# Kernel tuning notes

Measured on AMD Instinct MI355X. Metric: run time of the kernel, lower is better.

Reference implementation:

```python
import jax, jax.numpy as jnp
import numpy as np

T = 4096          # total tokens across ragged segments
H = 4096          # hidden_size
I = 11008         # intermediate_size
R = 16            # lora_rank
A = 4             # number of adapters (segments)


def setup_inputs() -> dict:
    key = jax.random.key(0)
    ks = jax.random.split(key, 12)
    inp = {
        "x": jax.random.normal(ks[0], (T, H), jnp.float32),
        "gate_w": jax.random.normal(ks[1], (I, H), jnp.float32) * (1.0 / np.sqrt(H)),
        "up_w": jax.random.normal(ks[2], (I, H), jnp.float32) * (1.0 / np.sqrt(H)),
        "down_w": jax.random.normal(ks[3], (H, I), jnp.float32) * (1.0 / np.sqrt(I)),
        "gate_wa": jax.random.normal(ks[4], (A, H, R), jnp.float32) * 0.01,
        "gate_wb": jax.random.normal(ks[5], (A, R, I), jnp.float32) * 0.01,
        "up_wa": jax.random.normal(ks[6], (A, H, R), jnp.float32) * 0.01,
        "up_wb": jax.random.normal(ks[7], (A, R, I), jnp.float32) * 0.01,
        "down_wa": jax.random.normal(ks[8], (A, I, R), jnp.float32) * 0.01,
        "down_wb": jax.random.normal(ks[9], (A, R, H), jnp.float32) * 0.01,
        "seg_ids": jnp.sort(jax.random.randint(ks[10], (T,), 0, A, jnp.int32)),
    }
    return inp


def _add_lora(y, inp, wa, wb, mask):
    # Segment-batched low-rank GEMM (Punica/S-LoRA add_lora):
    # for token t in segment a:  y[t] += inp[t] @ wa[a] @ wb[a]
    # mask: [T, A] one-hot of token->adapter assignment.
    # [A, T, R]: project into rank space for every adapter (R tiny), mask out
    xa = jnp.einsum('th,ahr->tar', inp, wa) * mask[:, :, None]   # [T, A, R]
    a, r = wb.shape[0], wb.shape[1]
    # collapse (A, R) so the expansion is one GEMM, no [A, T, out] intermediate
    delta = xa.reshape(inp.shape[0], a * r) @ wb.reshape(a * r, wb.shape[2])
    return y + delta


def reference(x, gate_w, up_w, down_w, gate_wa, gate_wb, up_wa, up_wb,
              down_wa, down_wb, seg_ids):
    mask = (seg_ids[:, None] == jnp.arange(A, dtype=seg_ids.dtype)[None, :]
            ).astype(x.dtype)                                    # [T, A]
    gate = x @ gate_w.T                                          # [T, I]
    gate = _add_lora(gate, x, gate_wa, gate_wb, mask)
    gate = jax.nn.silu(gate)
    up = x @ up_w.T                                              # [T, I]
    up = _add_lora(up, x, up_wa, up_wb, mask)
    t = gate * up
    down = t @ down_w.T                                          # [T, H]
    down = _add_lora(down, t, down_wa, down_wb, mask)
    return down
```

## Files before the change

kernel.cpp:

```cpp
#include <hip/hip_runtime.h>

#define T_TOK 4096
#define HID   4096
#define IMD   11008

using f32x4  = __attribute__((ext_vector_type(4))) float;
using bf16x8 = __attribute__((ext_vector_type(8))) __bf16;
union FragCast { int4 i; bf16x8 b; };

__device__ __forceinline__ unsigned f2bf_bits(float f) {
  unsigned u = __float_as_uint(f);
  return (u + 0x7fffu + ((u >> 16) & 1u)) >> 16;
}
__device__ __forceinline__ float bf2f(short s) {
  return __uint_as_float(((unsigned)(unsigned short)s) << 16);
}
__device__ __forceinline__ int4 cvt8(const float4 f0, const float4 f1) {
  int4 r;
  r.x = f2bf_bits(f0.x) | (f2bf_bits(f0.y) << 16);
  r.y = f2bf_bits(f0.z) | (f2bf_bits(f0.w) << 16);
  r.z = f2bf_bits(f1.x) | (f2bf_bits(f1.y) << 16);
  r.w = f2bf_bits(f1.z) | (f2bf_bits(f1.w) << 16);
  return r;
}
__device__ __forceinline__ void gload16(const void* g, void* l) {
  __builtin_amdgcn_global_load_lds(
      (__attribute__((address_space(1))) void*)g,
      (__attribute__((address_space(3))) void*)l, 16, 0, 0);
}

__global__ void cvt_pad(const float* __restrict__ in, short* __restrict__ out,
                        int C8, long ldin, long ldout) {
  long r = blockIdx.x;
  const float4* s = (const float4*)(in + r * ldin);
  int4* d = (int4*)(out + r * ldout);
  for (int c = threadIdx.x; c < C8; c += blockDim.x)
    d[c] = cvt8(s[2 * c], s[2 * c + 1]);
}

__global__ void build_wbT_pad(const float* __restrict__ wb,
                              short* __restrict__ out, int N, long ldout,
                              long K) {
  int n = blockIdx.x * blockDim.x + threadIdx.x;
  int ar = blockIdx.y;
  if (n < N) out[(long)n * ldout + K + ar] = (short)f2bf_bits(wb[(long)ar * N + n]);
}

__global__ void tail_copy(const short* __restrict__ src, short* dst, long ld) {
  dst[(long)blockIdx.x * ld + threadIdx.x] = src[blockIdx.x * 64 + threadIdx.x];
}

template <int KD, int NOUT>
__global__ __launch_bounds__(256)
void lora_proj(const short* __restrict__ Abf, long ldA,
               const float* __restrict__ wa0, const float* __restrict__ wa1,
               const int* __restrict__ seg, short* out0, long ld0, short* out1,
               long ld1) {
  __shared__ __align__(16) short rowbuf[KD];
  __shared__ float part[NOUT][4][16];
  int t = blockIdx.x, tid = threadIdx.x;
  int a = seg[t];
  const int4* src = (const int4*)(Abf + (long)t * ldA);
  for (int c = tid; c < KD / 8; c += 256) ((int4*)rowbuf)[c] = src[c];
  __syncthreads();
  int w = tid >> 6, l = tid & 63;
  int r = l & 15, g = l >> 4;
  const int HW = KD / 4;
  float s0 = 0.f, s1 = 0.f;
  const float* p0 = wa0 + (long)a * KD * 16 + r;
  const float* p1 = (NOUT == 2) ? (wa1 + (long)a * KD * 16 + r) : nullptr;
  int h = w * HW + g;
  for (int k = 0; k < HW / 4; ++k, h += 4) {
    float xv = bf2f(rowbuf[h]);
    s0 = fmaf(xv, p0[(long)h * 16], s0);
    if (NOUT == 2) s1 = fmaf(xv, p1[(long)h * 16], s1);
  }
  s0 += __shfl_xor(s0, 16); s0 += __shfl_xor(s0, 32);
  if (NOUT == 2) { s1 += __shfl_xor(s1, 16); s1 += __shfl_xor(s1, 32); }
  if (l < 16) { part[0][w][r] = s0; if (NOUT == 2) part[1][w][r] = s1; }
  __syncthreads();
  if (tid < 64 * NOUT) {
    int m = tid >> 6, ar = tid & 63;
    float v = 0.f;
    if ((ar >> 4) == a) {
      int r2 = ar & 15;
      v = part[m][0][r2] + part[m][1][r2] + part[m][2][r2] + part[m][3][r2];
    }
    short b = (short)f2bf_bits(v);
    if (m == 0) out0[(long)t * ld0 + ar] = b;
    else        out1[(long)t * ld1 + ar] = b;
  }
}

template <int MODE>
__global__ __launch_bounds__(512, 2)
void gemm256(const short* __restrict__ A, const short* __restrict__ B,
             const short* gbuf, short* outB, float* outF, int nby, long ldK,
             int iters, long ldo) {
  extern __shared__ __align__(16) char smem[];

  int nwg = gridDim.x;
  int orig = blockIdx.x;
  int q = nwg >> 3, rr = nwg & 7;
  int xcd = orig & 7, loc = orig >> 3;
  int swz = (xcd < rr ? xcd * (q + 1) : rr * (q + 1) + (xcd - rr) * q) + loc;
  int by = swz % nby, bx = swz / nby;
  long row0 = (long)bx * 256, col0 = (long)by * 256;

  int tid = threadIdx.x;
  int l = tid & 63, wid = tid >> 6;
  int wr = wid >> 2, wc = wid & 3;
  int lrow = l & 15, lhi = l >> 4, md = lrow & 7;

  const short* aP[4]; const short* bP[4];
  int dst[4];
#pragma unroll
  for (int k = 0; k < 4; ++k) {
    int idx = tid + k * 512;
    int r = idx >> 3, c8 = idx & 7;
    aP[k] = A + (row0 + r) * ldK + (c8 ^ (r & 7)) * 8;
    bP[k] = B + (col0 + r) * ldK + (c8 ^ (r & 7)) * 8;
    dst[k] = idx * 16;
  }

  auto stageA = [&](int bi) {
    char* d = smem + bi * 32768;
#pragma unroll
    for (int k = 0; k < 4; ++k) { gload16(aP[k], d + dst[k]); aP[k] += 64; }
  };
  auto stageB = [&](int bi) {
    char* d = smem + 98304 + bi * 32768;
#pragma unroll
    for (int k = 0; k < 4; ++k) { gload16(bP[k], d + dst[k]); bP[k] += 64; }
  };

  f32x4 acc[8][4];
  f32x4 zr = {0.f, 0.f, 0.f, 0.f};
#pragma unroll
  for (int mi = 0; mi < 8; ++mi)
#pragma unroll
    for (int ni = 0; ni < 4; ++ni) acc[mi][ni] = zr;

  const int csel0 = (lhi ^ md) * 16;
  const int csel1 = ((4 + lhi) ^ md) * 16;

  stageA(0); stageB(0); stageA(1);
  int ca = 0, sa = 2;
  for (int t = 0; t < iters; ++t) {
    if (t + 1 < iters) asm volatile("s_waitcnt vmcnt(4)" ::: "memory");
    else               asm volatile("s_waitcnt vmcnt(0)" ::: "memory");
    asm volatile("s_barrier" ::: "memory");
    if (t + 1 < iters) stageB((t + 1) & 1);
    if (t + 2 < iters) { stageA(sa); sa = (sa == 2) ? 0 : sa + 1; }

    const char* Ab = smem + ca * 32768;
    const char* Bb = smem + 98304 + (t & 1) * 32768;
    ca = (ca == 2) ? 0 : ca + 1;

    bf16x8 bF[4][2];
#pragma unroll
    for (int ni = 0; ni < 4; ++ni) {
      const char* base = Bb + (wc * 64 + ni * 16 + lrow) * 128;
      FragCast f0, f1;
      f0.i = *(const int4*)(base + csel0);
      f1.i = *(const int4*)(base + csel1);
      bF[ni][0] = f0.b; bF[ni][1] = f1.b;
    }
#pragma unroll
    for (int qm = 0; qm < 2; ++qm) {
      bf16x8 aF[4][2];
#pragma unroll
      for (int mi = 0; mi < 4; ++mi) {
        const char* base = Ab + (wr * 128 + qm * 64 + mi * 16 + lrow) * 128;
        FragCast f0, f1;
        f0.i = *(const int4*)(base + csel0);
        f1.i = *(const int4*)(base + csel1);
        aF[mi][0] = f0.b; aF[mi][1] = f1.b;
      }
      __builtin_amdgcn_s_setprio(1);
#pragma unroll
      for (int mi = 0; mi < 4; ++mi)
#pragma unroll
        for (int ni = 0; ni < 4; ++ni) {
          acc[qm * 4 + mi][ni] = __builtin_amdgcn_mfma_f32_16x16x32_bf16(
              aF[mi][0], bF[ni][0], acc[qm * 4 + mi][ni], 0, 0, 0);
          acc[qm * 4 + mi][ni] = __builtin_amdgcn_mfma_f32_16x16x32_bf16(
              aF[mi][1], bF[ni][1], acc[qm * 4 + mi][ni], 0, 0, 0);
        }
      __builtin_amdgcn_s_setprio(0);
    }
  }

#pragma unroll
  for (int qm = 0; qm < 2; ++qm)
#pragma unroll
    for (int mi = 0; mi < 4; ++mi)
#pragma unroll
      for (int ni = 0; ni < 4; ++ni)
#pragma unroll
        for (int j = 0; j < 4; ++j) {
          long grow = row0 + wr * 128 + qm * 64 + mi * 16 + lhi * 4 + j;
          long gcol = col0 + wc * 64 + ni * 16 + lrow;
          long idx = grow * ldo + gcol;
          float v = acc[qm * 4 + mi][ni][j];
          if constexpr (MODE == 0) {
            outB[idx] = (short)f2bf_bits(v);
          } else if constexpr (MODE == 1) {
            float g = bf2f(gbuf[idx]);
            float t2 = g * (1.f / (1.f + __expf(-g))) * v;
            outB[idx] = (short)f2bf_bits(t2);
          } else {
            outF[idx] = v;
          }
        }
}

extern "C" void kernel_launch(void* const* d_in, const int* in_sizes, int n_in,
                              void* d_out, int out_size, void* d_ws,
                              size_t ws_size, hipStream_t stream) {
  const float* x       = (const float*)d_in[0];
  const float* gate_w  = (const float*)d_in[1];
  const float* up_w    = (const float*)d_in[2];
  const float* down_w  = (const float*)d_in[3];
  const float* gate_wa = (const float*)d_in[4];
  const float* gate_wb = (const float*)d_in[5];
  const float* up_wa   = (const float*)d_in[6];
  const float* up_wb   = (const float*)d_in[7];
  const float* down_wa = (const float*)d_in[8];
  const float* down_wb = (const float*)d_in[9];
  const int*   seg     = (const int*)d_in[10];

  char* ws = (char*)d_ws;
  short* xg_pad = (short*)(ws);
  short* wA     = (short*)(ws + 34078720);
  short* wB     = (short*)(ws + 125665280);
  short* t_pad  = (short*)(ws + 217251840);
  short* xa_u   = (short*)(ws + 307953664);

  const int LDS_BYTES = 163840;
  hipFuncSetAttribute(reinterpret_cast<const void*>(&gemm256<0>),
                      hipFuncAttributeMaxDynamicSharedMemorySize, LDS_BYTES);
  hipFuncSetAttribute(reinterpret_cast<const void*>(&gemm256<1>),
                      hipFuncAttributeMaxDynamicSharedMemorySize, LDS_BYTES);
  hipFuncSetAttribute(reinterpret_cast<const void*>(&gemm256<2>),
                      hipFuncAttributeMaxDynamicSharedMemorySize, LDS_BYTES);

  cvt_pad<<<T_TOK, 256, 0, stream>>>(x, xg_pad, 512, HID, 4160);
  cvt_pad<<<IMD, 256, 0, stream>>>(gate_w, wA, 512, HID, 4160);
  cvt_pad<<<IMD, 256, 0, stream>>>(up_w, wB, 512, HID, 4160);
  build_wbT_pad<<<dim3(43, 64), 256, 0, stream>>>(gate_wb, wA, IMD, 4160, HID);
  build_wbT_pad<<<dim3(43, 64), 256, 0, stream>>>(up_wb, wB, IMD, 4160, HID);
  lora_proj<HID, 2><<<T_TOK, 256, 0, stream>>>(
      xg_pad, 4160, gate_wa, up_wa, seg, xg_pad + HID, 4160, xa_u, 64);

  gemm256<0><<<16 * 43, 512, LDS_BYTES, stream>>>(
      xg_pad, wA, nullptr, t_pad, nullptr, 43, 4160, 65, 11072);
  tail_copy<<<T_TOK, 64, 0, stream>>>(xa_u, xg_pad + HID, 4160);
  gemm256<1><<<16 * 43, 512, LDS_BYTES, stream>>>(
      xg_pad, wB, t_pad, t_pad, nullptr, 43, 4160, 65, 11072);

  cvt_pad<<<T_TOK, 256, 0, stream>>>(down_w, wA, 1376, IMD, 11072);
  build_wbT_pad<<<dim3(16, 64), 256, 0, stream>>>(down_wb, wA, HID, 11072, IMD);
  lora_proj<IMD, 1><<<T_TOK, 256, 0, stream>>>(
      t_pad, 11072, down_wa, nullptr, seg, t_pad + IMD, 11072, nullptr, 64);

  gemm256<2><<<16 * 16, 512, LDS_BYTES, stream>>>(
      t_pad, wA, nullptr, nullptr, (float*)d_out, 16, 11072, 173, 4096);
}
```

Measured before the change: 1.719 ms.

## Keep A operand in registers, persistent XCD-grouped tiles, drop tail copy

The GEMM is restructured so each wave loads its A fragments straight from global memory into registers, and only B is staged through LDS with triple buffering. LDS use drops to 96KB. The kernel becomes persistent: 256 workgroups loop over tiles grouped per XCD to improve L2 reuse. The gate and up LoRA columns are packed into a wider padded K (4224), which removes the tail_copy kernel and its shared xa buffer. The cost is heavier register pressure and A loads with global latency on the critical path.

```diff
diff --git a/kernel.cpp b/kernel.cpp
--- a/kernel.cpp
+++ b/kernel.cpp
@@ -30,12 +30,12 @@
 }
 
 __global__ void cvt_pad(const float* __restrict__ in, short* __restrict__ out,
-                        int C8, long ldin, long ldout) {
+                        int C8, int CT, long ldin, long ldout) {
   long r = blockIdx.x;
   const float4* s = (const float4*)(in + r * ldin);
   int4* d = (int4*)(out + r * ldout);
-  for (int c = threadIdx.x; c < C8; c += blockDim.x)
-    d[c] = cvt8(s[2 * c], s[2 * c + 1]);
+  for (int c = threadIdx.x; c < CT; c += blockDim.x)
+    d[c] = (c < C8) ? cvt8(s[2 * c], s[2 * c + 1]) : int4{0, 0, 0, 0};
 }
 
 __global__ void build_wbT_pad(const float* __restrict__ wb,
@@ -44,10 +44,6 @@
   int n = blockIdx.x * blockDim.x + threadIdx.x;
   int ar = blockIdx.y;
   if (n < N) out[(long)n * ldout + K + ar] = (short)f2bf_bits(wb[(long)ar * N + n]);
-}
-
-__global__ void tail_copy(const short* __restrict__ src, short* dst, long ld) {
-  dst[(long)blockIdx.x * ld + threadIdx.x] = src[blockIdx.x * 64 + threadIdx.x];
 }
 
 template <int KD, int NOUT>
@@ -92,117 +88,121 @@
   }
 }
 
-template <int MODE>
+template <int MODE, int ORDER>
 __global__ __launch_bounds__(512, 2)
-void gemm256(const short* __restrict__ A, const short* __restrict__ B,
-             const short* gbuf, short* outB, float* outF, int nby, long ldK,
-             int iters, long ldo) {
+void gemm_areg(const short* __restrict__ A, const short* __restrict__ B,
+               const short* __restrict__ gbuf, short* __restrict__ outB,
+               float* __restrict__ outF, int tilesPerXcd, long ldK, int iters,
+               long ldo) {
   extern __shared__ __align__(16) char smem[];
 
-  int nwg = gridDim.x;
-  int orig = blockIdx.x;
-  int q = nwg >> 3, rr = nwg & 7;
-  int xcd = orig & 7, loc = orig >> 3;
-  int swz = (xcd < rr ? xcd * (q + 1) : rr * (q + 1) + (xcd - rr) * q) + loc;
-  int by = swz % nby, bx = swz / nby;
-  long row0 = (long)bx * 256, col0 = (long)by * 256;
-
+  int xcd = blockIdx.x & 7, loc = blockIdx.x >> 3;
   int tid = threadIdx.x;
   int l = tid & 63, wid = tid >> 6;
   int wr = wid >> 2, wc = wid & 3;
   int lrow = l & 15, lhi = l >> 4, md = lrow & 7;
 
-  const short* aP[4]; const short* bP[4];
-  int dst[4];
-#pragma unroll
-  for (int k = 0; k < 4; ++k) {
-    int idx = tid + k * 512;
-    int r = idx >> 3, c8 = idx & 7;
-    aP[k] = A + (row0 + r) * ldK + (c8 ^ (r & 7)) * 8;
-    bP[k] = B + (col0 + r) * ldK + (c8 ^ (r & 7)) * 8;
-    dst[k] = idx * 16;
-  }
-
-  auto stageA = [&](int bi) {
-    char* d = smem + bi * 32768;
-#pragma unroll
-    for (int k = 0; k < 4; ++k) { gload16(aP[k], d + dst[k]); aP[k] += 64; }
+  const int rr0 = tid >> 3, cc0 = tid & 7;
+  const long bOffC = (long)((cc0 ^ (rr0 & 7)) * 8);
+
+  long row0, col0;
+  const short* pB; const short* pA;
+  auto setTile = [&](int r) {
+    int gt = xcd * tilesPerXcd + r;
+    int t0 = gt & 15, t1 = gt >> 4;
+    int bx = (ORDER == 1) ? t0 : t1;
+    int by = (ORDER == 1) ? t1 : t0;
+    row0 = (long)bx * 256; col0 = (long)by * 256;
+    pB = B + (col0 + rr0) * ldK + bOffC;
+    pA = A + (row0 + wr * 128 + lrow) * ldK + lhi * 8;
   };
-  auto stageB = [&](int bi) {
-    char* d = smem + 98304 + bi * 32768;
-#pragma unroll
-    for (int k = 0; k < 4; ++k) { gload16(bP[k], d + dst[k]); bP[k] += 64; }
+
+  auto stB = [&](int slot, int kt) {
+    char* d = smem + slot * 32768 + tid * 16;
+    const short* s = pB + (long)kt * 64;
+    gload16(s, d);
+    gload16(s + (long)64 * ldK, d + 8192);
+    gload16(s + (long)128 * ldK, d + 16384);
+    gload16(s + (long)192 * ldK, d + 24576);
   };
 
-  f32x4 acc[8][4];
+  FragCast aR[8][2];
+  bf16x8 bF[4][2];
+  auto readB = [&](int slot) {
+#pragma unroll
+    for (int ni = 0; ni < 4; ++ni) {
+      const char* base = smem + slot * 32768 + (wc * 64 + ni * 16 + lrow) * 128;
+      FragCast f0, f1;
+      f0.i = *(const int4*)(base + ((lhi) ^ md) * 16);
+      f1.i = *(const int4*)(base + ((4 + lhi) ^ md) * 16);
+      bF[ni][0] = f0.b; bF[ni][1] = f1.b;
+    }
+  };
+
   f32x4 zr = {0.f, 0.f, 0.f, 0.f};
-#pragma unroll
-  for (int mi = 0; mi < 8; ++mi)
-#pragma unroll
-    for (int ni = 0; ni < 4; ++ni) acc[mi][ni] = zr;
-
-  const int csel0 = (lhi ^ md) * 16;
-  const int csel1 = ((4 + lhi) ^ md) * 16;
-
-  stageA(0); stageB(0); stageA(1);
-  int ca = 0, sa = 2;
-  for (int t = 0; t < iters; ++t) {
-    if (t + 1 < iters) asm volatile("s_waitcnt vmcnt(4)" ::: "memory");
-    else               asm volatile("s_waitcnt vmcnt(0)" ::: "memory");
+
+  int r = loc;
+  bool first = true;
+  while (r < tilesPerXcd) {
+    setTile(r);
+    stB(0, 0); stB(1, 1);
+#pragma unroll
+    for (int mi = 0; mi < 8; ++mi) {
+      const short* s = pA + (long)mi * 16 * ldK;
+      aR[mi][0].i = *(const int4*)s;
+      aR[mi][1].i = *(const int4*)(s + 32);
+    }
+    asm volatile("s_waitcnt vmcnt(20)" ::: "memory");
     asm volatile("s_barrier" ::: "memory");
-    if (t + 1 < iters) stageB((t + 1) & 1);
-    if (t + 2 < iters) { stageA(sa); sa = (sa == 2) ? 0 : sa + 1; }
-
-    const char* Ab = smem + ca * 32768;
-    const char* Bb = smem + 98304 + (t & 1) * 32768;
-    ca = (ca == 2) ? 0 : ca + 1;
-
-    bf16x8 bF[4][2];
-#pragma unroll
-    for (int ni = 0; ni < 4; ++ni) {
-      const char* base = Bb + (wc * 64 + ni * 16 + lrow) * 128;
-      FragCast f0, f1;
-      f0.i = *(const int4*)(base + csel0);
-      f1.i = *(const int4*)(base + csel1);
-      bF[ni][0] = f0.b; bF[ni][1] = f1.b;
-    }
-#pragma unroll
-    for (int qm = 0; qm < 2; ++qm) {
-      bf16x8 aF[4][2];
-#pragma unroll
-      for (int mi = 0; mi < 4; ++mi) {
-        const char* base = Ab + (wr * 128 + qm * 64 + mi * 16 + lrow) * 128;
-        FragCast f0, f1;
-        f0.i = *(const int4*)(base + csel0);
-        f1.i = *(const int4*)(base + csel1);
-        aF[mi][0] = f0.b; aF[mi][1] = f1.b;
+    (void)first; first = false;
+
+    f32x4 acc[8][4];
+#pragma unroll
+    for (int mi = 0; mi < 8; ++mi)
+#pragma unroll
+      for (int ni = 0; ni < 4; ++ni) acc[mi][ni] = zr;
+
+    int cur = 0;
+#pragma unroll 1
+    for (int t = 0; t < iters; ++t) {
+      readB(cur);
+      int st2 = (cur >= 1) ? cur - 1 : 2;
+      if (t + 2 < iters) stB(st2, t + 2);
+      __builtin_amdgcn_s_setprio(1);
+#pragma unroll
+      for (int mi = 0; mi < 8; ++mi) {
+#pragma unroll
+        for (int ni = 0; ni < 4; ++ni) {
+          acc[mi][ni] = __builtin_amdgcn_mfma_f32_16x16x32_bf16(
+              aR[mi][0].b, bF[ni][0], acc[mi][ni], 0, 0, 0);
+          acc[mi][ni] = __builtin_amdgcn_mfma_f32_16x16x32_bf16(
+              aR[mi][1].b, bF[ni][1], acc[mi][ni], 0, 0, 0);
+        }
+        if (t + 1 < iters) {
+          const short* s = pA + (long)mi * 16 * ldK + (long)(t + 1) * 64;
+          aR[mi][0].i = *(const int4*)s;
+          aR[mi][1].i = *(const int4*)(s + 32);
+        }
       }
-      __builtin_amdgcn_s_setprio(1);
-#pragma unroll
-      for (int mi = 0; mi < 4; ++mi)
-#pragma unroll
-        for (int ni = 0; ni < 4; ++ni) {
-          acc[qm * 4 + mi][ni] = __builtin_amdgcn_mfma_f32_16x16x32_bf16(
-              aF[mi][0], bF[ni][0], acc[qm * 4 + mi][ni], 0, 0, 0);
-          acc[qm * 4 + mi][ni] = __builtin_amdgcn_mfma_f32_16x16x32_bf16(
-              aF[mi][1], bF[ni][1], acc[qm * 4 + mi][ni], 0, 0, 0);
-        }
       __builtin_amdgcn_s_setprio(0);
-    }
-  }
-
-#pragma unroll
-  for (int qm = 0; qm < 2; ++qm)
-#pragma unroll
-    for (int mi = 0; mi < 4; ++mi)
+      if (t + 1 < iters) {
+        if (t + 2 < iters) asm volatile("s_waitcnt vmcnt(20)" ::: "memory");
+        else               asm volatile("s_waitcnt vmcnt(16)" ::: "memory");
+        asm volatile("s_barrier" ::: "memory");
+      }
+      cur = (cur == 2) ? 0 : cur + 1;
+    }
+
+#pragma unroll
+    for (int mi = 0; mi < 8; ++mi)
 #pragma unroll
       for (int ni = 0; ni < 4; ++ni)
 #pragma unroll
         for (int j = 0; j < 4; ++j) {
-          long grow = row0 + wr * 128 + qm * 64 + mi * 16 + lhi * 4 + j;
+          long grow = row0 + wr * 128 + mi * 16 + lhi * 4 + j;
           long gcol = col0 + wc * 64 + ni * 16 + lrow;
           long idx = grow * ldo + gcol;
-          float v = acc[qm * 4 + mi][ni][j];
+          float v = acc[mi][ni][j];
           if constexpr (MODE == 0) {
             outB[idx] = (short)f2bf_bits(v);
           } else if constexpr (MODE == 1) {
@@ -213,6 +213,8 @@
             outF[idx] = v;
           }
         }
+    r += 32;
+  }
 }
 
 extern "C" void kernel_launch(void* const* d_in, const int* in_sizes, int n_in,
@@ -232,38 +234,38 @@
 
   char* ws = (char*)d_ws;
   short* xg_pad = (short*)(ws);
-  short* wA     = (short*)(ws + 34078720);
-  short* wB     = (short*)(ws + 125665280);
-  short* t_pad  = (short*)(ws + 217251840);
-  short* xa_u   = (short*)(ws + 307953664);
-
-  const int LDS_BYTES = 163840;
-  hipFuncSetAttribute(reinterpret_cast<const void*>(&gemm256<0>),
-                      hipFuncAttributeMaxDynamicSharedMemorySize, LDS_BYTES);
-  hipFuncSetAttribute(reinterpret_cast<const void*>(&gemm256<1>),
-                      hipFuncAttributeMaxDynamicSharedMemorySize, LDS_BYTES);
-  hipFuncSetAttribute(reinterpret_cast<const void*>(&gemm256<2>),
-                      hipFuncAttributeMaxDynamicSharedMemorySize, LDS_BYTES);
-
-  cvt_pad<<<T_TOK, 256, 0, stream>>>(x, xg_pad, 512, HID, 4160);
-  cvt_pad<<<IMD, 256, 0, stream>>>(gate_w, wA, 512, HID, 4160);
-  cvt_pad<<<IMD, 256, 0, stream>>>(up_w, wB, 512, HID, 4160);
-  build_wbT_pad<<<dim3(43, 64), 256, 0, stream>>>(gate_wb, wA, IMD, 4160, HID);
-  build_wbT_pad<<<dim3(43, 64), 256, 0, stream>>>(up_wb, wB, IMD, 4160, HID);
+  short* wA     = (short*)(ws + 34603008);
+  short* wB     = (short*)(ws + 127598592);
+  short* t_pad  = (short*)(ws + 220594176);
+
+  const int LDS_B = 98304;
+  hipFuncSetAttribute(reinterpret_cast<const void*>(&gemm_areg<0, 1>),
+                      hipFuncAttributeMaxDynamicSharedMemorySize, LDS_B);
+  hipFuncSetAttribute(reinterpret_cast<const void*>(&gemm_areg<1, 1>),
+                      hipFuncAttributeMaxDynamicSharedMemorySize, LDS_B);
+  hipFuncSetAttribute(reinterpret_cast<const void*>(&gemm_areg<2, 0>),
+                      hipFuncAttributeMaxDynamicSharedMemorySize, LDS_B);
+
+  cvt_pad<<<T_TOK, 256, 0, stream>>>(x, xg_pad, 512, 512, HID, 4224);
+  cvt_pad<<<IMD, 256, 0, stream>>>(gate_w, wA, 512, 528, HID, 4224);
+  cvt_pad<<<IMD, 256, 0, stream>>>(up_w, wB, 512, 528, HID, 4224);
+  build_wbT_pad<<<dim3(43, 64), 256, 0, stream>>>(gate_wb, wA, IMD, 4224, 4096);
+  build_wbT_pad<<<dim3(43, 64), 256, 0, stream>>>(up_wb, wB, IMD, 4224, 4160);
   lora_proj<HID, 2><<<T_TOK, 256, 0, stream>>>(
-      xg_pad, 4160, gate_wa, up_wa, seg, xg_pad + HID, 4160, xa_u, 64);
-
-  gemm256<0><<<16 * 43, 512, LDS_BYTES, stream>>>(
-      xg_pad, wA, nullptr, t_pad, nullptr, 43, 4160, 65, 11072);
-  tail_copy<<<T_TOK, 64, 0, stream>>>(xa_u, xg_pad + HID, 4160);
-  gemm256<1><<<16 * 43, 512, LDS_BYTES, stream>>>(
-      xg_pad, wB, t_pad, t_pad, nullptr, 43, 4160, 65, 11072);
-
-  cvt_pad<<<T_TOK, 256, 0, stream>>>(down_w, wA, 1376, IMD, 11072);
-  build_wbT_pad<<<dim3(16, 64), 256, 0, stream>>>(down_wb, wA, HID, 11072, IMD);
+      xg_pad, 4224, gate_wa, up_wa, seg, xg_pad + 4096, 4224, xg_pad + 4160,
+      4224);
+
+  gemm_areg<0, 1><<<256, 512, LDS_B, stream>>>(
+      xg_pad, wA, nullptr, t_pad, nullptr, 86, 4224, 66, 11072);
+  gemm_areg<1, 1><<<256, 512, LDS_B, stream>>>(
+      xg_pad, wB, t_pad, t_pad, nullptr, 86, 4224, 66, 11072);
+
+  cvt_pad<<<T_TOK, 256, 0, stream>>>(down_w, wA, 1376, 1376, IMD, 11072);
+  build_wbT_pad<<<dim3(16, 64), 256, 0, stream>>>(down_wb, wA, HID, 11072,
+                                                  IMD);
   lora_proj<IMD, 1><<<T_TOK, 256, 0, stream>>>(
       t_pad, 11072, down_wa, nullptr, seg, t_pad + IMD, 11072, nullptr, 64);
 
-  gemm256<2><<<16 * 16, 512, LDS_BYTES, stream>>>(
-      t_pad, wA, nullptr, nullptr, (float*)d_out, 16, 11072, 173, 4096);
-}
+  gemm_areg<2, 0><<<256, 512, LDS_B, stream>>>(
+      t_pad, wA, nullptr, nullptr, (float*)d_out, 32, 11072, 173, 4096);
+}
```

After: 2.995 ms. +74.3%, slower.
